# Kernel optimization log

Measured on AMD Instinct MI355X. Metric: run time of the kernel, lower is better.

## Reference

```python
import jax, jax.numpy as jnp
import numpy as np

B, M, D, H, DH = 8, 1024, 768, 12, 64
R, RF, RW, DFF = 32, 384, 384, 3072
EPS = 1e-12  # BERT LayerNorm eps


def _ln(z, g, b):
    mu = jnp.mean(z, -1, keepdims=True)
    var = jnp.mean((z - mu) ** 2, -1, keepdims=True)
    return g * (z - mu) * jax.lax.rsqrt(var + EPS) + b


def setup_inputs() -> dict:
    ks = jax.random.split(jax.random.key(0), 20)
    n = lambda k, s: jax.random.normal(k, s, dtype=jnp.float32) * 0.02
    return {
        "x": jax.random.normal(ks[0], (B, M, D), dtype=jnp.float32),
        "mask": jnp.zeros((B, M), jnp.float32),  # additive attention mask
        "Pq": n(ks[1], (H, D, R)), "Vq": n(ks[2], (H, R, DH)), "bq": n(ks[3], (H, DH)),
        "Pk": n(ks[4], (H, D, R)), "Vk": n(ks[5], (H, R, DH)), "bk": n(ks[6], (H, DH)),
        "Pv": n(ks[7], (H, D, R)), "Vv": n(ks[8], (H, R, DH)), "bv": n(ks[9], (H, DH)),
        "Uo": n(ks[10], (D, RW)), "Vo": n(ks[11], (RW, D)), "bo_attn": n(ks[12], (D,)),
        "U1": n(ks[13], (D, RF)), "V1": n(ks[14], (RF, DFF)), "b1": n(ks[15], (DFF,)),
        "U2": n(ks[16], (DFF, RF)), "V2": n(ks[17], (RF, D)), "b2": n(ks[18], (D,)),
        "ln1_g": jnp.ones((D,), jnp.float32), "ln1_b": jnp.zeros((D,), jnp.float32),
        "ln2_g": jnp.ones((D,), jnp.float32), "ln2_b": jnp.zeros((D,), jnp.float32),
    }


def reference(x, mask, Pq, Vq, bq, Pk, Vk, bk, Pv, Vv, bv, Uo, Vo, bo_attn,
              U1, V1, b1, U2, V2, b2, ln1_g, ln1_b, ln2_g, ln2_b):
    Bx, Mx, dm = x.shape
    dh = dm // Pq.shape[0]
    scale = 1.0 / (dh ** 0.5)
    # low-rank per-head Q/K/V: x @ P (d->r) then @ V (r->dh), + per-head bias
    Q = jnp.einsum('bmd,hdr,hrk->bhmk', x, Pq, Vq) + bq[None, :, None, :]
    K = jnp.einsum('bmd,hdr,hrk->bhmk', x, Pk, Vk) + bk[None, :, None, :]
    V = jnp.einsum('bmd,hdr,hrk->bhmk', x, Pv, Vv) + bv[None, :, None, :]
    scores = jnp.einsum('bhmk,bhnk->bhmn', Q, K) * scale + mask[:, None, None, :]
    probs = jax.nn.softmax(scores, axis=-1)
    attn = jnp.einsum('bhmn,bhnk->bhmk', probs, V)
    attn = attn.transpose(0, 2, 1, 3).reshape(Bx, Mx, dm)  # (B, M, d_model)
    # low-rank attention output projection + residual + LN1
    x1 = _ln(x + (attn @ Uo) @ Vo + bo_attn, ln1_g, ln1_b)
    # low-rank FFN: GELU((x1 @ U1) @ V1 + b1) @ U2 @ V2 + b2 (BERT exact gelu)
    mid = x1 @ U1
    y = (jax.nn.gelu(mid @ V1 + b1, approximate=False) @ U2) @ V2 + b2
    return _ln(x1 + y, ln2_g, ln2_b)
```

## Files before the change

### kernel.cpp

```cpp
#include <hip/hip_runtime.h>
#include <cstddef>

#define D_MODEL 768
#define NHEAD   12
#define DHEAD   64
#define RANK    32
#define SEQ     1024
#define BATCH   8
#define BM      8192

typedef __attribute__((ext_vector_type(8))) short short8;
typedef __attribute__((ext_vector_type(4))) float floatx4;

__device__ inline ushort f2b(float f) {
  union { float f; unsigned u; } v; v.f = f;
  unsigned r = v.u + 0x7fffu + ((v.u >> 16) & 1u);
  return (ushort)(r >> 16);
}
__device__ inline float b2f(ushort h) {
  union { unsigned u; float f; } v; v.u = ((unsigned)h) << 16;
  return v.f;
}
__device__ inline unsigned pk2(float a, float b) {
  return ((__float_as_uint(b) + 0x8000u) & 0xffff0000u) |
         ((__float_as_uint(a) + 0x8000u) >> 16);
}
__device__ inline float fast_gelu(float x) {
  float z = 0.79788456080286536f * (x + 0.044715f * x * x * x);
  float e = __expf(2.f * z);
  float t = 1.f - 2.f / (e + 1.f);
  return 0.5f * x * (1.f + t);
}

__global__ __launch_bounds__(256) void f2b_kernel(
    const float* __restrict__ in, ushort* __restrict__ out, int n) {
  int i = (blockIdx.x * 256 + threadIdx.x) * 4;
  if (i >= n) return;
  float4 v = *(const float4*)(in + i);
  ushort4 o;
  o.x = f2b(v.x); o.y = f2b(v.y); o.z = f2b(v.z); o.w = f2b(v.w);
  *(ushort4*)(out + i) = o;
}

__global__ __launch_bounds__(256) void combine_qkv_kernel(
    const float* __restrict__ Pq, const float* __restrict__ Vq,
    const float* __restrict__ Pk, const float* __restrict__ Vk,
    const float* __restrict__ Pv, const float* __restrict__ Vv,
    ushort* __restrict__ Wt) {
  int which = blockIdx.y;
  const float* P  = which == 0 ? Pq : (which == 1 ? Pk : Pv);
  const float* Vw = which == 0 ? Vq : (which == 1 ? Vk : Vv);
  ushort* W = Wt + (size_t)which * D_MODEL * D_MODEL;
  int idx = blockIdx.x * 256 + threadIdx.x;
  if (idx >= D_MODEL * NHEAD * DHEAD) return;
  int c = idx / D_MODEL;
  int d = idx - c * D_MODEL;
  int h = c >> 6, k = c & 63;
  const float* p = P + ((size_t)h * D_MODEL + d) * RANK;
  const float* v = Vw + (size_t)h * RANK * DHEAD + k;
  float s = 0.f;
#pragma unroll
  for (int r = 0; r < RANK; r++) s += p[r] * v[(size_t)r * DHEAD];
  W[(size_t)c * D_MODEL + d] = f2b(s);
}

__global__ __launch_bounds__(256) void concat_bias_kernel(
    const float* __restrict__ bq, const float* __restrict__ bk,
    const float* __restrict__ bv, float* __restrict__ out) {
  int i = blockIdx.x * 256 + threadIdx.x;
  if (i >= 2304) return;
  out[i] = (i < 768) ? bq[i] : (i < 1536 ? bk[i - 768] : bv[i - 1536]);
}

__global__ __launch_bounds__(256) void prep_weights_kernel(
    const float* __restrict__ U1, const float* __restrict__ V1,
    const float* __restrict__ U2, const float* __restrict__ V2,
    const float* __restrict__ Vo, const float* __restrict__ Uo,
    ushort* __restrict__ U1t, ushort* __restrict__ V1t,
    ushort* __restrict__ U2t, ushort* __restrict__ V2t,
    ushort* __restrict__ VoT, ushort* __restrict__ Uob) {
  __shared__ float t[32][33];
  int blk = blockIdx.x;
  if (blk >= 3168) {
    int i = (blk - 3168) * 1024 + threadIdx.x * 4;
    float4 v = *(const float4*)(Uo + i);
    ushort4 o;
    o.x = f2b(v.x); o.y = f2b(v.y); o.z = f2b(v.z); o.w = f2b(v.w);
    *(ushort4*)(Uob + i) = o;
    return;
  }
  const float* in; ushort* out; int R, C, bx, by;
  if (blk < 288)       { in = U1; out = U1t; R = 768;  C = 384;  int i = blk;        bx = i % 12; by = i / 12; }
  else if (blk < 1440) { in = V1; out = V1t; R = 384;  C = 3072; int i = blk - 288;  bx = i % 96; by = i / 96; }
  else if (blk < 2592) { in = U2; out = U2t; R = 3072; C = 384;  int i = blk - 1440; bx = i % 12; by = i / 12; }
  else if (blk < 2880) { in = V2; out = V2t; R = 384;  C = 768;  int i = blk - 2592; bx = i % 24; by = i / 24; }
  else                 { in = Vo; out = VoT; R = 384;  C = 768;  int i = blk - 2880; bx = i % 24; by = i / 24; }
  int c0 = bx * 32, r0 = by * 32;
  int lx = threadIdx.x & 31, ly = threadIdx.x >> 5;
#pragma unroll
  for (int i = 0; i < 32; i += 8)
    t[ly + i][lx] = in[(size_t)(r0 + ly + i) * C + c0 + lx];
  __syncthreads();
#pragma unroll
  for (int i = 0; i < 32; i += 8)
    out[(size_t)(c0 + ly + i) * R + r0 + lx] = f2b(t[lx][ly + i]);
}

template <int OUTMODE, int BIAS, int GELU>
__global__ __launch_bounds__(256) void gemm_mfma_kernel(
    const ushort* __restrict__ A, const ushort* __restrict__ Bt,
    const float* __restrict__ bias, void* __restrict__ C,
    void* __restrict__ C2, void* __restrict__ C3,
    int M, int N, int K) {
  __shared__ __align__(16) ushort Als[128 * 32];
  __shared__ __align__(16) ushort Bls[128 * 32];
  const int tid  = threadIdx.x;
  const int lane = tid & 63;
  const int quad = lane >> 4, l16 = lane & 15;
  const int wu   = __builtin_amdgcn_readfirstlane(tid >> 6);
  const int wrow = (wu >> 1) * 64, wcol = (wu & 1) * 64;
  const int row0 = blockIdx.y * 128, col0 = blockIdx.x * 128;

  floatx4 acc[4][4] = {};

  for (int k0 = 0; k0 < K; k0 += 32) {
    __syncthreads();
#pragma unroll
    for (int is = 0; is < 2; is++) {
      int c = is * 256 + wu * 64 + lane;
      int m = c >> 2, kk = (c & 3) << 3;
      const ushort* ga = A + (size_t)(row0 + m) * K + (k0 + kk);
      ushort* la = Als + (size_t)(is * 256 + wu * 64) * 8;
      __builtin_amdgcn_global_load_lds(
          (const __attribute__((address_space(1))) void*)ga,
          (__attribute__((address_space(3))) void*)la, 16, 0, 0);
      const ushort* gb = Bt + (size_t)(col0 + m) * K + (k0 + kk);
      ushort* lb = Bls + (size_t)(is * 256 + wu * 64) * 8;
      __builtin_amdgcn_global_load_lds(
          (const __attribute__((address_space(1))) void*)gb,
          (__attribute__((address_space(3))) void*)lb, 16, 0, 0);
    }
    __syncthreads();

    short8 af[4], bf[4];
#pragma unroll
    for (int mt = 0; mt < 4; mt++)
      af[mt] = *(const short8*)(Als + ((wrow + mt * 16 + l16) * 32 + quad * 8));
#pragma unroll
    for (int nt = 0; nt < 4; nt++)
      bf[nt] = *(const short8*)(Bls + ((wcol + nt * 16 + l16) * 32 + quad * 8));
#pragma unroll
    for (int mt = 0; mt < 4; mt++)
#pragma unroll
      for (int nt = 0; nt < 4; nt++)
        acc[mt][nt] = __builtin_amdgcn_mfma_f32_16x16x32_bf16(
            af[mt], bf[nt], acc[mt][nt], 0, 0, 0);
  }

#pragma unroll
  for (int mt = 0; mt < 4; mt++) {
#pragma unroll
    for (int nt = 0; nt < 4; nt++) {
      int colg = col0 + wcol + nt * 16 + l16;
      float bv_ = BIAS ? bias[colg] : 0.f;
      float v4[4];
#pragma unroll
      for (int r = 0; r < 4; r++) {
        float v = acc[mt][nt][r] + bv_;
        if (GELU) v = fast_gelu(v);
        v4[r] = v;
      }
      int rowg0 = row0 + wrow + mt * 16 + quad * 4;
      if (OUTMODE == 3) {
        int seg = col0 / 768;
        int cl = colg - seg * 768;
        if (seg == 2) {
          ushort4 o;
          o.x = f2b(v4[0]); o.y = f2b(v4[1]); o.z = f2b(v4[2]); o.w = f2b(v4[3]);
          *(ushort4*)((ushort*)C3 + (size_t)cl * BM + rowg0) = o;
        } else {
          ushort* dst = (seg == 0) ? (ushort*)C : (ushort*)C2;
          float sc = (seg == 0) ? 0.125f : 1.f;
#pragma unroll
          for (int r = 0; r < 4; r++)
            dst[(size_t)(rowg0 + r) * D_MODEL + cl] = f2b(v4[r] * sc);
        }
      } else {
#pragma unroll
        for (int r = 0; r < 4; r++)
          ((ushort*)C)[(size_t)(rowg0 + r) * N + colg] = f2b(v4[r]);
      }
    }
  }
}

template <int BIAS>
__global__ __launch_bounds__(256) void gemm_n64_kernel(
    const ushort* __restrict__ A, const ushort* __restrict__ Bt,
    const float* __restrict__ bias, ushort* __restrict__ C,
    int M, int N, int K) {
  __shared__ __align__(16) ushort Als[128 * 32];
  __shared__ __align__(16) ushort Bls[64 * 32];
  const int tid  = threadIdx.x;
  const int lane = tid & 63;
  const int quad = lane >> 4, l16 = lane & 15;
  const int wu   = __builtin_amdgcn_readfirstlane(tid >> 6);
  const int row0 = blockIdx.y * 128, col0 = blockIdx.x * 64;

  floatx4 acc[2][4] = {};

  for (int k0 = 0; k0 < K; k0 += 32) {
    __syncthreads();
#pragma unroll
    for (int is = 0; is < 2; is++) {
      int c = is * 256 + wu * 64 + lane;
      int m = c >> 2, kk = (c & 3) << 3;
      const ushort* ga = A + (size_t)(row0 + m) * K + (k0 + kk);
      ushort* la = Als + (size_t)(is * 256 + wu * 64) * 8;
      __builtin_amdgcn_global_load_lds(
          (const __attribute__((address_space(1))) void*)ga,
          (__attribute__((address_space(3))) void*)la, 16, 0, 0);
    }
    {
      int c = wu * 64 + lane;
      int m = c >> 2, kk = (c & 3) << 3;
      const ushort* gb = Bt + (size_t)(col0 + m) * K + (k0 + kk);
      ushort* lb = Bls + (size_t)(wu * 64) * 8;
      __builtin_amdgcn_global_load_lds(
          (const __attribute__((address_space(1))) void*)gb,
          (__attribute__((address_space(3))) void*)lb, 16, 0, 0);
    }
    __syncthreads();

    short8 af[2], bf[4];
#pragma unroll
    for (int mt = 0; mt < 2; mt++)
      af[mt] = *(const short8*)(Als + ((wu * 32 + mt * 16 + l16) * 32 + quad * 8));
#pragma unroll
    for (int nt = 0; nt < 4; nt++)
      bf[nt] = *(const short8*)(Bls + ((nt * 16 + l16) * 32 + quad * 8));
#pragma unroll
    for (int mt = 0; mt < 2; mt++)
#pragma unroll
      for (int nt = 0; nt < 4; nt++)
        acc[mt][nt] = __builtin_amdgcn_mfma_f32_16x16x32_bf16(
            af[mt], bf[nt], acc[mt][nt], 0, 0, 0);
  }

#pragma unroll
  for (int mt = 0; mt < 2; mt++) {
#pragma unroll
    for (int nt = 0; nt < 4; nt++) {
      int colg = col0 + nt * 16 + l16;
      float bv_ = BIAS ? bias[colg] : 0.f;
      int rowg0 = row0 + wu * 32 + mt * 16 + quad * 4;
#pragma unroll
      for (int r = 0; r < 4; r++)
        C[(size_t)(rowg0 + r) * N + colg] = f2b(acc[mt][nt][r] + bv_);
    }
  }
}

__global__ __launch_bounds__(256) void gemm_mfma_splitk_kernel(
    const ushort* __restrict__ A, const ushort* __restrict__ Bt,
    float* __restrict__ Cpart, int M, int N, int Ktot, int Kper) {
  __shared__ __align__(16) ushort Als[128 * 32];
  __shared__ __align__(16) ushort Bls[128 * 32];
  const int tid  = threadIdx.x;
  const int lane = tid & 63;
  const int quad = lane >> 4, l16 = lane & 15;
  const int wu   = __builtin_amdgcn_readfirstlane(tid >> 6);
  const int wrow = (wu >> 1) * 64, wcol = (wu & 1) * 64;
  const int row0 = blockIdx.y * 128, col0 = blockIdx.x * 128;
  const int kbase = blockIdx.z * Kper;
  float* Cz = Cpart + (size_t)blockIdx.z * M * N;

  floatx4 acc[4][4] = {};

  for (int k0 = kbase; k0 < kbase + Kper; k0 += 32) {
    __syncthreads();
#pragma unroll
    for (int is = 0; is < 2; is++) {
      int c = is * 256 + wu * 64 + lane;
      int m = c >> 2, kk = (c & 3) << 3;
      const ushort* ga = A + (size_t)(row0 + m) * Ktot + (k0 + kk);
      ushort* la = Als + (size_t)(is * 256 + wu * 64) * 8;
      __builtin_amdgcn_global_load_lds(
          (const __attribute__((address_space(1))) void*)ga,
          (__attribute__((address_space(3))) void*)la, 16, 0, 0);
      const ushort* gb = Bt + (size_t)(col0 + m) * Ktot + (k0 + kk);
      ushort* lb = Bls + (size_t)(is * 256 + wu * 64) * 8;
      __builtin_amdgcn_global_load_lds(
          (const __attribute__((address_space(1))) void*)gb,
          (__attribute__((address_space(3))) void*)lb, 16, 0, 0);
    }
    __syncthreads();

    short8 af[4], bf[4];
#pragma unroll
    for (int mt = 0; mt < 4; mt++)
      af[mt] = *(const short8*)(Als + ((wrow + mt * 16 + l16) * 32 + quad * 8));
#pragma unroll
    for (int nt = 0; nt < 4; nt++)
      bf[nt] = *(const short8*)(Bls + ((wcol + nt * 16 + l16) * 32 + quad * 8));
#pragma unroll
    for (int mt = 0; mt < 4; mt++)
#pragma unroll
      for (int nt = 0; nt < 4; nt++)
        acc[mt][nt] = __builtin_amdgcn_mfma_f32_16x16x32_bf16(
            af[mt], bf[nt], acc[mt][nt], 0, 0, 0);
  }

#pragma unroll
  for (int mt = 0; mt < 4; mt++)
#pragma unroll
    for (int nt = 0; nt < 4; nt++) {
      int colg = col0 + wcol + nt * 16 + l16;
      int rowg0 = row0 + wrow + mt * 16 + quad * 4;
#pragma unroll
      for (int r = 0; r < 4; r++)
        Cz[(size_t)(rowg0 + r) * N + colg] = acc[mt][nt][r];
    }
}

__global__ __launch_bounds__(256) void reduce_splitk_kernel(
    const float* __restrict__ part, ushort* __restrict__ out, int n, int S) {
  int i = (blockIdx.x * 256 + threadIdx.x) * 4;
  if (i >= n) return;
  float4 a = *(const float4*)(part + i);
  for (int s = 1; s < S; s++) {
    float4 b = *(const float4*)(part + (size_t)s * n + i);
    a.x += b.x; a.y += b.y; a.z += b.z; a.w += b.w;
  }
  ushort4 o;
  o.x = f2b(a.x); o.y = f2b(a.y); o.z = f2b(a.z); o.w = f2b(a.w);
  *(ushort4*)(out + i) = o;
}

__global__ __launch_bounds__(256, 3) void attn_mfma_kernel(
    const ushort* __restrict__ Q, const ushort* __restrict__ K,
    const ushort* __restrict__ Vt, const float* __restrict__ mask,
    ushort* __restrict__ O) {
  const int bid  = blockIdx.x;
  const int xcd  = bid & 7;
  const int rest = bid >> 3;
  const int qt   = rest & 7;
  const int grp  = (rest >> 3) * 8 + xcd;
  const int h = grp % 12, b = grp / 12;

  const int tid = threadIdx.x;
  const int lane = tid & 63;
  const int quad = lane >> 4, l16 = lane & 15;
  const int wu = __builtin_amdgcn_readfirstlane(tid >> 6);
  const int qrow0 = qt * 128 + wu * 32;

  __shared__ __align__(16) ushort Ks[128 * 72];
  __shared__ __align__(16) ushort Vts[64 * 136];
  __shared__ __align__(16) float Msk[128];

  short8 qf[2][2];
#pragma unroll
  for (int rt = 0; rt < 2; rt++) {
    const ushort* qp = Q + ((size_t)(b * SEQ + qrow0 + rt * 16 + l16)) * D_MODEL
                     + h * DHEAD + quad * 8;
    qf[rt][0] = *(const short8*)qp;
    qf[rt][1] = *(const short8*)(qp + 32);
  }

  const int j0 = tid >> 3, gk = (tid & 7) * 8;
  const int d0 = tid >> 4, gv = (tid & 15) * 8;
  const ushort* Kg = K + ((size_t)(b * SEQ + j0)) * D_MODEL + h * DHEAD + gk;
  const ushort* Vg = Vt + ((size_t)(h * DHEAD + d0)) * BM + b * SEQ + gv;
  ushort* Kl = Ks + j0 * 72 + gk;
  ushort* Vl = Vts + d0 * 136 + gv;

  short8 kst[4], vst[4];
#pragma unroll
  for (int p = 0; p < 4; p++)
    kst[p] = *(const short8*)(Kg + (size_t)p * (32 * D_MODEL));
#pragma unroll
  for (int p = 0; p < 4; p++)
    vst[p] = *(const short8*)(Vg + (size_t)p * (16 * BM));

  float lsum[2] = {0.f, 0.f};
  floatx4 o_acc[2][4] = {};
  const int base01 = (((quad & 1) << 5) | l16) << 2;
  const bool lotile = (quad < 2);

  for (int n0 = 0; n0 < SEQ; n0 += 128) {
    asm volatile("" ::: "memory");
    __builtin_amdgcn_s_barrier();
    asm volatile("" ::: "memory");

#pragma unroll
    for (int p = 0; p < 4; p++) *(short8*)(Kl + p * (32 * 72)) = kst[p];
#pragma unroll
    for (int p = 0; p < 4; p++) *(short8*)(Vl + p * (16 * 136)) = vst[p];

    if (tid < 128) Msk[tid] = mask[(size_t)b * SEQ + n0 + tid];
    asm volatile("" ::: "memory");

    if (n0 + 128 < SEQ) {
#pragma unroll
      for (int p = 0; p < 4; p++)
        kst[p] = *(const short8*)(Kg + (size_t)(n0 + 128) * D_MODEL
                                     + (size_t)p * (32 * D_MODEL));
#pragma unroll
      for (int p = 0; p < 4; p++)
        vst[p] = *(const short8*)(Vg + (n0 + 128) + (size_t)p * (16 * BM));
    }

    asm volatile("s_waitcnt lgkmcnt(0)" ::: "memory");
    __builtin_amdgcn_s_barrier();
    asm volatile("" ::: "memory");

    unsigned UA[2][8], UB[2][8];
#pragma unroll
    for (int ct = 0; ct < 8; ct++) {
      short8 ka = *(const short8*)(Ks + (ct * 16 + l16) * 72 + quad * 8);
      short8 kb = *(const short8*)(Ks + (ct * 16 + l16) * 72 + 32 + quad * 8);
      float4 mk = *(const float4*)(Msk + ct * 16 + quad * 4);
#pragma unroll
      for (int rt = 0; rt < 2; rt++) {
        floatx4 st = {};
        st = __builtin_amdgcn_mfma_f32_16x16x32_bf16(ka, qf[rt][0], st, 0, 0, 0);
        st = __builtin_amdgcn_mfma_f32_16x16x32_bf16(kb, qf[rt][1], st, 0, 0, 0);
        float e0 = __expf(st[0] + mk.x);
        float e1 = __expf(st[1] + mk.y);
        float e2 = __expf(st[2] + mk.z);
        float e3 = __expf(st[3] + mk.w);
        lsum[rt] += (e0 + e1) + (e2 + e3);
        UA[rt][ct] = pk2(e0, e1);
        UB[rt][ct] = pk2(e2, e3);
      }
    }

#pragma unroll
    for (int kk = 0; kk < 4; kk++) {
      short8 pa[2];
#pragma unroll
      for (int rt = 0; rt < 2; rt++) {
        int a0 = __builtin_amdgcn_ds_bpermute(base01, (int)UA[rt][2 * kk]);
        int a1 = __builtin_amdgcn_ds_bpermute(base01, (int)UA[rt][2 * kk + 1]);
        int b0 = __builtin_amdgcn_ds_bpermute(base01, (int)UB[rt][2 * kk]);
        int b1 = __builtin_amdgcn_ds_bpermute(base01, (int)UB[rt][2 * kk + 1]);
        int c0 = __builtin_amdgcn_ds_bpermute(base01 + 64, (int)UA[rt][2 * kk]);
        int c1 = __builtin_amdgcn_ds_bpermute(base01 + 64, (int)UA[rt][2 * kk + 1]);
        int d0_ = __builtin_amdgcn_ds_bpermute(base01 + 64, (int)UB[rt][2 * kk]);
        int d1 = __builtin_amdgcn_ds_bpermute(base01 + 64, (int)UB[rt][2 * kk + 1]);
        int4 t;
        t.x = lotile ? a0 : a1;
        t.y = lotile ? b0 : b1;
        t.z = lotile ? c0 : c1;
        t.w = lotile ? d0_ : d1;
        pa[rt] = *(short8*)&t;
      }
#pragma unroll
      for (int dt = 0; dt < 4; dt++) {
        short8 vb = *(const short8*)(Vts + (dt * 16 + l16) * 136 + kk * 32 + quad * 8);
#pragma unroll
        for (int rt = 0; rt < 2; rt++)
          o_acc[rt][dt] = __builtin_amdgcn_mfma_f32_16x16x32_bf16(pa[rt], vb, o_acc[rt][dt], 0, 0, 0);
      }
    }
  }

#pragma unroll
  for (int rt = 0; rt < 2; rt++) {
    float l = lsum[rt];
    l += __shfl_xor(l, 16);
    l += __shfl_xor(l, 32);
    float inv = 1.f / l;
    int lanebase = lane & 48;
#pragma unroll
    for (int rr = 0; rr < 4; rr++) {
      int iv = __builtin_amdgcn_ds_bpermute((lanebase | (quad * 4 + rr)) << 2,
                                            __float_as_int(inv));
      float invr = __int_as_float(iv);
      size_t rowg = (size_t)(b * SEQ + qrow0 + rt * 16 + quad * 4 + rr);
#pragma unroll
      for (int dt = 0; dt < 4; dt++)
        O[rowg * D_MODEL + h * DHEAD + dt * 16 + l16] = f2b(o_acc[rt][dt][rr] * invr);
    }
  }
}

template <int AIN_BF16, int OUT_FP32, int OUT_BF16>
__global__ __launch_bounds__(256) void add_ln_kernel(
    const float* __restrict__ Ainf, const ushort* __restrict__ Ainb,
    const ushort* __restrict__ Binb,
    const float* __restrict__ g, const float* __restrict__ bt,
    float* __restrict__ outf, ushort* __restrict__ outb) {
  const int row = blockIdx.x, tid = threadIdx.x;
  __shared__ float red[4];
  float v[3];
  float s = 0.f;
#pragma unroll
  for (int u = 0; u < 3; u++) {
    int c = tid + u * 256;
    float a = AIN_BF16 ? b2f(Ainb[(size_t)row * 768 + c]) : Ainf[(size_t)row * 768 + c];
    v[u] = a + b2f(Binb[(size_t)row * 768 + c]);
    s += v[u];
  }
#pragma unroll
  for (int off = 32; off > 0; off >>= 1) s += __shfl_down(s, off);
  if ((tid & 63) == 0) red[tid >> 6] = s;
  __syncthreads();
  float mu = (red[0] + red[1] + red[2] + red[3]) * (1.f / 768.f);
  float s2 = 0.f;
#pragma unroll
  for (int u = 0; u < 3; u++) { float d = v[u] - mu; s2 += d * d; }
#pragma unroll
  for (int off = 32; off > 0; off >>= 1) s2 += __shfl_down(s2, off);
  __syncthreads();
  if ((tid & 63) == 0) red[tid >> 6] = s2;
  __syncthreads();
  float var = (red[0] + red[1] + red[2] + red[3]) * (1.f / 768.f);
  float inv = rsqrtf(var + 1e-12f);
#pragma unroll
  for (int u = 0; u < 3; u++) {
    int c = tid + u * 256;
    float r = g[c] * (v[u] - mu) * inv + bt[c];
    if (OUT_FP32) outf[(size_t)row * 768 + c] = r;
    if (OUT_BF16) outb[(size_t)row * 768 + c] = f2b(r);
  }
}

extern "C" void kernel_launch(void* const* d_in, const int* in_sizes, int n_in,
                              void* d_out, int out_size, void* d_ws, size_t ws_size,
                              hipStream_t stream) {
  const float* x    = (const float*)d_in[0];
  const float* mask = (const float*)d_in[1];
  const float* Pq   = (const float*)d_in[2];
  const float* Vq   = (const float*)d_in[3];
  const float* bq   = (const float*)d_in[4];
  const float* Pk   = (const float*)d_in[5];
  const float* Vk   = (const float*)d_in[6];
  const float* bk   = (const float*)d_in[7];
  const float* Pv   = (const float*)d_in[8];
  const float* Vv   = (const float*)d_in[9];
  const float* bv   = (const float*)d_in[10];
  const float* Uo   = (const float*)d_in[11];
  const float* Vo   = (const float*)d_in[12];
  const float* bo   = (const float*)d_in[13];
  const float* U1   = (const float*)d_in[14];
  const float* V1   = (const float*)d_in[15];
  const float* b1   = (const float*)d_in[16];
  const float* U2   = (const float*)d_in[17];
  const float* V2   = (const float*)d_in[18];
  const float* b2   = (const float*)d_in[19];
  const float* g1   = (const float*)d_in[20];
  const float* be1  = (const float*)d_in[21];
  const float* g2   = (const float*)d_in[22];
  const float* be2  = (const float*)d_in[23];

  char* w = (char*)d_ws;
  auto alloc = [&](size_t bytes) -> char* {
    char* p = w; w += (bytes + 255) & ~(size_t)255; return p;
  };
  ushort* xb     = (ushort*)alloc((size_t)BM * 768 * 2);
  ushort* Wqkvt  = (ushort*)alloc((size_t)2304 * 768 * 2);
  float*  ball   = (float*)alloc(2304 * 4);
  ushort* VoT    = (ushort*)alloc(768 * 384 * 2);
  ushort* Uob    = (ushort*)alloc(768 * 384 * 2);
  ushort* Wot    = (ushort*)alloc(768 * 768 * 2);
  ushort* U1t    = (ushort*)alloc(384 * 768 * 2);
  ushort* V1t    = (ushort*)alloc((size_t)3072 * 384 * 2);
  ushort* U2t    = (ushort*)alloc((size_t)384 * 3072 * 2);
  ushort* V2t    = (ushort*)alloc(768 * 384 * 2);
  ushort* Qb     = (ushort*)alloc((size_t)BM * 768 * 2);
  ushort* Kb     = (ushort*)alloc((size_t)BM * 768 * 2);
  ushort* Vtb    = (ushort*)alloc((size_t)768 * BM * 2);
  ushort* attnb  = (ushort*)alloc((size_t)BM * 768 * 2);
  ushort* mtb    = (ushort*)alloc((size_t)BM * 384 * 2);
  ushort* y1b    = (ushort*)alloc((size_t)BM * 768 * 2);
  ushort* x1b    = (ushort*)alloc((size_t)BM * 768 * 2);
  float*  part   = (float*)alloc((size_t)4 * BM * 384 * 4);
  ushort* hiddenb = Qb;
  ushort* y2b     = y1b;
  float*  outp    = (float*)d_out;

  f2b_kernel<<<(BM * 768) / 1024, 256, 0, stream>>>(x, xb, BM * 768);
  combine_qkv_kernel<<<dim3(2304, 3), 256, 0, stream>>>(Pq, Vq, Pk, Vk, Pv, Vv, Wqkvt);
  concat_bias_kernel<<<9, 256, 0, stream>>>(bq, bk, bv, ball);
  prep_weights_kernel<<<3456, 256, 0, stream>>>(U1, V1, U2, V2, Vo, Uo,
                                                U1t, V1t, U2t, V2t, VoT, Uob);
  gemm_n64_kernel<0><<<dim3(12, 6), 256, 0, stream>>>(VoT, Uob, nullptr, Wot, 768, 768, 384);

  gemm_mfma_kernel<3, 1, 0><<<dim3(18, 64), 256, 0, stream>>>(
      xb, Wqkvt, ball, Qb, Kb, Vtb, BM, 2304, 768);

  attn_mfma_kernel<<<dim3(768), 256, 0, stream>>>(Qb, Kb, Vtb, mask, attnb);

  gemm_n64_kernel<1><<<dim3(12, 64), 256, 0, stream>>>(attnb, Wot, bo, y1b, BM, 768, 768);
  add_ln_kernel<0, 0, 1><<<BM, 256, 0, stream>>>(x, nullptr, y1b, g1, be1, nullptr, x1b);

  gemm_mfma_splitk_kernel<<<dim3(3, 64, 4), 256, 0, stream>>>(
      x1b, U1t, part, BM, 384, 768, 192);
  reduce_splitk_kernel<<<(BM * 384) / 1024, 256, 0, stream>>>(part, mtb, BM * 384, 4);
  gemm_mfma_kernel<1, 1, 1><<<dim3(24, 64), 256, 0, stream>>>(
      mtb, V1t, b1, hiddenb, nullptr, nullptr, BM, 3072, 384);
  gemm_mfma_splitk_kernel<<<dim3(3, 64, 4), 256, 0, stream>>>(
      hiddenb, U2t, part, BM, 384, 3072, 768);
  reduce_splitk_kernel<<<(BM * 384) / 1024, 256, 0, stream>>>(part, mtb, BM * 384, 4);
  gemm_n64_kernel<1><<<dim3(12, 64), 256, 0, stream>>>(mtb, V2t, b2, y2b, BM, 768, 384);

  add_ln_kernel<1, 1, 0><<<BM, 256, 0, stream>>>(nullptr, x1b, y2b, g2, be2, outp, nullptr);
}
```

Measured before the change: 456.6 us.

## Load attention K/V fragments directly from global and use permlane swaps

```diff
diff --git a/kernel.cpp b/kernel.cpp
--- a/kernel.cpp
+++ b/kernel.cpp
@@ -354,10 +354,6 @@
   const int wu = __builtin_amdgcn_readfirstlane(tid >> 6);
   const int qrow0 = qt * 128 + wu * 32;
 
-  __shared__ __align__(16) ushort Ks[128 * 72];
-  __shared__ __align__(16) ushort Vts[64 * 136];
-  __shared__ __align__(16) float Msk[128];
-
   short8 qf[2][2];
 #pragma unroll
   for (int rt = 0; rt < 2; rt++) {
@@ -367,59 +363,21 @@
     qf[rt][1] = *(const short8*)(qp + 32);
   }
 
-  const int j0 = tid >> 3, gk = (tid & 7) * 8;
-  const int d0 = tid >> 4, gv = (tid & 15) * 8;
-  const ushort* Kg = K + ((size_t)(b * SEQ + j0)) * D_MODEL + h * DHEAD + gk;
-  const ushort* Vg = Vt + ((size_t)(h * DHEAD + d0)) * BM + b * SEQ + gv;
-  ushort* Kl = Ks + j0 * 72 + gk;
-  ushort* Vl = Vts + d0 * 136 + gv;
-
-  short8 kst[4], vst[4];
-#pragma unroll
-  for (int p = 0; p < 4; p++)
-    kst[p] = *(const short8*)(Kg + (size_t)p * (32 * D_MODEL));
-#pragma unroll
-  for (int p = 0; p < 4; p++)
-    vst[p] = *(const short8*)(Vg + (size_t)p * (16 * BM));
+  const ushort* Kp = K + ((size_t)(b * SEQ + l16)) * D_MODEL + h * DHEAD + quad * 8;
+  const ushort* Vp = Vt + ((size_t)(h * DHEAD + l16)) * BM + b * SEQ + quad * 8;
+  const float*  Mp = mask + (size_t)b * SEQ + quad * 4;
 
   float lsum[2] = {0.f, 0.f};
   floatx4 o_acc[2][4] = {};
-  const int base01 = (((quad & 1) << 5) | l16) << 2;
-  const bool lotile = (quad < 2);
 
   for (int n0 = 0; n0 < SEQ; n0 += 128) {
-    asm volatile("" ::: "memory");
-    __builtin_amdgcn_s_barrier();
-    asm volatile("" ::: "memory");
-
-#pragma unroll
-    for (int p = 0; p < 4; p++) *(short8*)(Kl + p * (32 * 72)) = kst[p];
-#pragma unroll
-    for (int p = 0; p < 4; p++) *(short8*)(Vl + p * (16 * 136)) = vst[p];
-
-    if (tid < 128) Msk[tid] = mask[(size_t)b * SEQ + n0 + tid];
-    asm volatile("" ::: "memory");
-
-    if (n0 + 128 < SEQ) {
-#pragma unroll
-      for (int p = 0; p < 4; p++)
-        kst[p] = *(const short8*)(Kg + (size_t)(n0 + 128) * D_MODEL
-                                     + (size_t)p * (32 * D_MODEL));
-#pragma unroll
-      for (int p = 0; p < 4; p++)
-        vst[p] = *(const short8*)(Vg + (n0 + 128) + (size_t)p * (16 * BM));
-    }
-
-    asm volatile("s_waitcnt lgkmcnt(0)" ::: "memory");
-    __builtin_amdgcn_s_barrier();
-    asm volatile("" ::: "memory");
-
     unsigned UA[2][8], UB[2][8];
 #pragma unroll
     for (int ct = 0; ct < 8; ct++) {
-      short8 ka = *(const short8*)(Ks + (ct * 16 + l16) * 72 + quad * 8);
-      short8 kb = *(const short8*)(Ks + (ct * 16 + l16) * 72 + 32 + quad * 8);
-      float4 mk = *(const float4*)(Msk + ct * 16 + quad * 4);
+      const ushort* kp = Kp + (size_t)(n0 + ct * 16) * D_MODEL;
+      short8 ka = *(const short8*)kp;
+      short8 kb = *(const short8*)(kp + 32);
+      float4 mk = *(const float4*)(Mp + n0 + ct * 16);
 #pragma unroll
       for (int rt = 0; rt < 2; rt++) {
         floatx4 st = {};
@@ -440,24 +398,22 @@
       short8 pa[2];
 #pragma unroll
       for (int rt = 0; rt < 2; rt++) {
-        int a0 = __builtin_amdgcn_ds_bpermute(base01, (int)UA[rt][2 * kk]);
-        int a1 = __builtin_amdgcn_ds_bpermute(base01, (int)UA[rt][2 * kk + 1]);
-        int b0 = __builtin_amdgcn_ds_bpermute(base01, (int)UB[rt][2 * kk]);
-        int b1 = __builtin_amdgcn_ds_bpermute(base01, (int)UB[rt][2 * kk + 1]);
-        int c0 = __builtin_amdgcn_ds_bpermute(base01 + 64, (int)UA[rt][2 * kk]);
-        int c1 = __builtin_amdgcn_ds_bpermute(base01 + 64, (int)UA[rt][2 * kk + 1]);
-        int d0_ = __builtin_amdgcn_ds_bpermute(base01 + 64, (int)UB[rt][2 * kk]);
-        int d1 = __builtin_amdgcn_ds_bpermute(base01 + 64, (int)UB[rt][2 * kk + 1]);
+        unsigned a0 = UA[rt][2 * kk], a2 = UA[rt][2 * kk + 1];
+        unsigned b1 = UB[rt][2 * kk], b3 = UB[rt][2 * kk + 1];
+        asm("v_permlane32_swap_b32 %0, %1" : "+v"(a0), "+v"(a2));
+        asm("v_permlane16_swap_b32 %0, %1" : "+v"(a0), "+v"(a2));
+        asm("v_permlane32_swap_b32 %0, %1" : "+v"(b1), "+v"(b3));
+        asm("v_permlane16_swap_b32 %0, %1" : "+v"(b1), "+v"(b3));
         int4 t;
-        t.x = lotile ? a0 : a1;
-        t.y = lotile ? b0 : b1;
-        t.z = lotile ? c0 : c1;
-        t.w = lotile ? d0_ : d1;
+        t.x = (int)a0;
+        t.y = (int)b1;
+        t.z = (int)a2;
+        t.w = (int)b3;
         pa[rt] = *(short8*)&t;
       }
 #pragma unroll
       for (int dt = 0; dt < 4; dt++) {
-        short8 vb = *(const short8*)(Vts + (dt * 16 + l16) * 136 + kk * 32 + quad * 8);
+        short8 vb = *(const short8*)(Vp + (size_t)(dt * 16) * BM + n0 + kk * 32);
 #pragma unroll
         for (int rt = 0; rt < 2; rt++)
           o_acc[rt][dt] = __builtin_amdgcn_mfma_f32_16x16x32_bf16(pa[rt], vb, o_acc[rt][dt], 0, 0, 0);
```

After: 495.4 us. 1.08x slower.
